# Performance work log

Measured on AMD Instinct MI355X. Metric: run time of the kernel, lower is better.

The kernel has to match this reference:

```python
import jax, jax.numpy as jnp
import numpy as np

N_NODES = 50000
N_EDGES = 1600000
D_IN = 128
D_HID = 256   # 2 * input_dims
FC1 = 256
FC2 = 256
N_ACT = 8
EPS = 1e-5


def layer_norm(x, w, b):
    mu = jnp.mean(x, axis=-1, keepdims=True)
    var = jnp.mean((x - mu) ** 2, axis=-1, keepdims=True)
    return (x - mu) * jax.lax.rsqrt(var + EPS) * w + b


def setup_inputs() -> dict:
    key = jax.random.key(0)
    ks = jax.random.split(key, 16)
    state = jax.random.normal(ks[0], (N_NODES, D_IN), dtype=jnp.float32)
    edge_index = jax.random.randint(ks[1], (2, N_EDGES), 0, N_NODES, dtype=jnp.int64)
    agent_i = 7
    # GCNConv params (glorot-ish init is fine for a numeric reference)
    conv_w = jax.random.normal(ks[2], (D_IN, D_HID), dtype=jnp.float32) / np.sqrt(D_IN)
    conv_b = jnp.zeros((D_HID,), dtype=jnp.float32)
    f1 = 1.0 / np.sqrt(D_HID)
    fc1_w = jax.random.uniform(ks[3], (D_HID, FC1), minval=-f1, maxval=f1, dtype=jnp.float32)
    fc1_b = jax.random.uniform(ks[4], (FC1,), minval=-f1, maxval=f1, dtype=jnp.float32)
    f2 = 1.0 / np.sqrt(FC1)
    fc2_w = jax.random.uniform(ks[5], (FC1, FC2), minval=-f2, maxval=f2, dtype=jnp.float32)
    fc2_b = jax.random.uniform(ks[6], (FC2,), minval=-f2, maxval=f2, dtype=jnp.float32)
    ln1_w = jnp.ones((FC1,), dtype=jnp.float32)
    ln1_b = jnp.zeros((FC1,), dtype=jnp.float32)
    ln2_w = jnp.ones((FC2,), dtype=jnp.float32)
    ln2_b = jnp.zeros((FC2,), dtype=jnp.float32)
    f3 = 0.003
    mu_w = jax.random.uniform(ks[7], (FC2, N_ACT), minval=-f3, maxval=f3, dtype=jnp.float32)
    mu_b = jax.random.uniform(ks[8], (N_ACT,), minval=-f3, maxval=f3, dtype=jnp.float32)
    return {
        "state": state, "edge_index": edge_index, "agent_i": agent_i,
        "conv_w": conv_w, "conv_b": conv_b,
        "fc1_w": fc1_w, "fc1_b": fc1_b, "ln1_w": ln1_w, "ln1_b": ln1_b,
        "fc2_w": fc2_w, "fc2_b": fc2_b, "ln2_w": ln2_w, "ln2_b": ln2_b,
        "mu_w": mu_w, "mu_b": mu_b,
    }


def gcn_conv(x, edge_index, w, b):
    N = x.shape[0]
    loops = jnp.arange(N, dtype=edge_index.dtype)
    src = jnp.concatenate([edge_index[0], loops])
    dst = jnp.concatenate([edge_index[1], loops])
    ones = jnp.ones(src.shape[0], dtype=x.dtype)
    deg = jax.ops.segment_sum(ones, dst, num_segments=N)
    dinv = jnp.where(deg > 0, jax.lax.rsqrt(deg), 0.0)
    norm = dinv[src] * dinv[dst]                        # [E+N]
    h = x @ w                                           # [N, D_HID]
    msg = h[src] * norm[:, None]                        # gather: [E+N, D_HID]
    return jax.ops.segment_sum(msg, dst, num_segments=N) + b


def reference(state, edge_index, agent_i, conv_w, conv_b,
              fc1_w, fc1_b, ln1_w, ln1_b, fc2_w, fc2_b, ln2_w, ln2_b,
              mu_w, mu_b):
    x = gcn_conv(state, edge_index, conv_w, conv_b)     # [N, D_HID]
    x = jax.nn.relu(x[agent_i])                         # [D_HID]
    x = jax.nn.relu(layer_norm(x @ fc1_w + fc1_b, ln1_w, ln1_b))
    x = jax.nn.relu(layer_norm(x @ fc2_w + fc2_b, ln2_w, ln2_b))
    return jax.nn.sigmoid(x @ mu_w + mu_b)              # [N_ACT]
```

## Files before the change

kernel.cpp:

```cpp
#include <hip/hip_runtime.h>
#include <hip/hip_bf16.h>

#define D_IN  128
#define D_HID 256
#define NB_A  256
#define NT_A  512
#define NB_B  256
#define NT_B  512
#define NT_C  512
#define MAXG  512
#define HASHN 2048
#define PBM_STRIDE 72

#define OFF_BAR  0
#define OFF_M    16
#define OFF_DEG  32
#define OFF_PBM  1024
#define OFF_CM   20480
#define OFF_MAP  21504
#define OFF_H0   24576
#define OFF_H1   25088
#define OFF_H2   25600

#define ALD(p)   __hip_atomic_load((p),      __ATOMIC_RELAXED, __HIP_MEMORY_SCOPE_AGENT)
#define AST(p,v) __hip_atomic_store((p),(v), __ATOMIC_RELAXED, __HIP_MEMORY_SCOPE_AGENT)

__device__ __forceinline__ float ldf(const void* p, long long i, bool b16) {
    if (b16) {
        unsigned short u = ((const unsigned short*)p)[i];
        return __uint_as_float(((unsigned int)u) << 16);
    }
    return ((const float*)p)[i];
}

__device__ __forceinline__ unsigned hash_n(int key) {
    return (((unsigned)key * 2654435761u) >> 21) & (HASHN - 1);
}

__device__ __forceinline__ int detect_i64(const void* edges, int tid, int* s) {
    if (tid < 64) {
        const unsigned* w = (const unsigned*)edges;
        unsigned long long b = __ballot(w[2 * tid + 1] == 0u);
        if (tid == 0) *s = (b == ~0ULL) ? 1 : 0;
    }
    __syncthreads();
    return *s;
}

__device__ __forceinline__ int detect_b16(const void* state, int tid, int* s) {
    if (tid < 64) {
        const unsigned short* p = (const unsigned short*)state;
        unsigned short v = p[tid];
        int e = (v >> 7) & 0xff;
        unsigned long long b = __ballot(v == 0 || (e >= 90 && e <= 140));
        if (tid == 0) *s = (b == ~0ULL) ? 1 : 0;
    }
    __syncthreads();
    return *s;
}

__device__ __forceinline__ void grid_bar(int* slot, int cnt, bool wait) {
    __syncthreads();
    if (threadIdx.x == 0) {
        __threadfence();
        __hip_atomic_fetch_add(slot, 1, __ATOMIC_RELEASE, __HIP_MEMORY_SCOPE_AGENT);
        if (wait) {
            while (__hip_atomic_load(slot, __ATOMIC_RELAXED, __HIP_MEMORY_SCOPE_AGENT) < cnt)
                __builtin_amdgcn_s_sleep(2);
            __threadfence();
        }
    }
    __syncthreads();
}

__global__ void __launch_bounds__(NT_A) k_A(const void* edges, const void* state,
                                            const int* agent_p,
                                            const void* w0, const void* w1,
                                            const void* w2, const void* w3,
                                            int* wsi, long long n_edges) {
    __shared__ int s_pref[NT_A];
    __shared__ int s_list[64];
    __shared__ int s_i64, s_b16;
    int tid = threadIdx.x, bid = blockIdx.x;
    int i64 = detect_i64(edges, tid, &s_i64);
    int b16 = detect_b16(state, tid, &s_b16);

    if (bid == 0) {
        if (tid < 8) AST(&wsi[OFF_BAR + tid], 0);
        for (int i = tid; i <= MAXG; i += NT_A) AST(&wsi[OFF_DEG + i], 0);
    }

    {
        int esz = b16 ? 2 : 4;
        long long gt = (long long)bid * NT_A + tid;
        const void* arr[4] = { w0, w1, w2, w3 };
        const int elems[4] = { D_IN * D_HID, D_HID * D_HID, D_HID * D_HID, D_HID * 8 };
        long long base = 0;
        #pragma unroll
        for (int a = 0; a < 4; a++) {
            long long lines = ((long long)elems[a] * esz) >> 6;
            long long idx = gt - base;
            if (idx >= 0 && idx < lines) {
                unsigned v = *(const unsigned*)((const char*)arr[a] + (idx << 6));
                asm volatile("" :: "v"(v));
            }
            base += lines;
        }
    }

    int agent = agent_p[0];
    long long base4 = ((long long)bid * NT_A + tid) * 4;
    const long long stride4 = (long long)NB_A * NT_A * 4;
    long long nv = n_edges & ~3LL;
    int c = 0;
    if (i64) {
        const long long* dst = (const long long*)edges + n_edges;
        for (long long e = base4; e < nv; e += stride4) {
            long2 a = *(const long2*)(dst + e);
            long2 b = *(const long2*)(dst + e + 2);
            c += ((int)a.x == agent) + ((int)a.y == agent)
               + ((int)b.x == agent) + ((int)b.y == agent);
        }
        if (bid == 0 && tid == 0)
            for (long long e = nv; e < n_edges; e++) c += ((int)dst[e] == agent);
    } else {
        const int* dst = (const int*)edges + n_edges;
        for (long long e = base4; e < nv; e += stride4) {
            int4 a = *(const int4*)(dst + e);
            c += (a.x == agent) + (a.y == agent) + (a.z == agent) + (a.w == agent);
        }
        if (bid == 0 && tid == 0)
            for (long long e = nv; e < n_edges; e++) c += (dst[e] == agent);
    }
    s_pref[tid] = c;
    __syncthreads();
    #pragma unroll
    for (int off = 1; off < NT_A; off <<= 1) {
        int v = (tid >= off) ? s_pref[tid - off] : 0;
        __syncthreads();
        s_pref[tid] += v;
        __syncthreads();
    }
    int excl = s_pref[tid] - c;
    int total = s_pref[NT_A - 1];
    if (c > 0 && excl < 64) {
        int k = excl;
        if (i64) {
            const long long* src = (const long long*)edges;
            const long long* dst = src + n_edges;
            for (long long e = base4; e < nv; e += stride4) {
                long2 a = *(const long2*)(dst + e);
                long2 b = *(const long2*)(dst + e + 2);
                if ((int)a.x == agent) { if (k < 64) s_list[k] = (int)src[e];     k++; }
                if ((int)a.y == agent) { if (k < 64) s_list[k] = (int)src[e + 1]; k++; }
                if ((int)b.x == agent) { if (k < 64) s_list[k] = (int)src[e + 2]; k++; }
                if ((int)b.y == agent) { if (k < 64) s_list[k] = (int)src[e + 3]; k++; }
            }
            if (bid == 0 && tid == 0)
                for (long long e = nv; e < n_edges; e++)
                    if ((int)dst[e] == agent) { if (k < 64) s_list[k] = (int)src[e]; k++; }
        } else {
            const int* src = (const int*)edges;
            const int* dst = src + n_edges;
            for (long long e = base4; e < nv; e += stride4) {
                int4 a = *(const int4*)(dst + e);
                if (a.x == agent) { if (k < 64) s_list[k] = src[e];     k++; }
                if (a.y == agent) { if (k < 64) s_list[k] = src[e + 1]; k++; }
                if (a.z == agent) { if (k < 64) s_list[k] = src[e + 2]; k++; }
                if (a.w == agent) { if (k < 64) s_list[k] = src[e + 3]; k++; }
            }
            if (bid == 0 && tid == 0)
                for (long long e = nv; e < n_edges; e++)
                    if (dst[e] == agent) { if (k < 64) s_list[k] = src[e]; k++; }
        }
    }
    __syncthreads();
    int* reg = wsi + OFF_PBM + bid * PBM_STRIDE;
    int tw = total < 64 ? total : 64;
    if (tid == 0) reg[0] = tw;
    if (tid < tw) reg[1 + tid] = s_list[tid];
}

__global__ void __launch_bounds__(NT_B) k_B(const void* edges, const int* agent_p,
                                            int* wsi, long long n_edges) {
    __shared__ int s_pref[NT_B];
    __shared__ int s_nodes[MAXG + 1];
    __shared__ int s_hkey[HASHN];
    __shared__ int s_hval[HASHN];
    __shared__ int s_cnt[MAXG + 1];
    __shared__ int s_i64, s_nu;
    int tid = threadIdx.x, bid = blockIdx.x;
    int i64 = detect_i64(edges, tid, &s_i64);

    int bc = 0;
    if (tid < NB_A) {
        bc = wsi[OFF_PBM + tid * PBM_STRIDE];
        bc = bc < 64 ? (bc < 0 ? 0 : bc) : 64;
    }
    s_pref[tid] = bc;
    __syncthreads();
    #pragma unroll
    for (int off = 1; off < NT_B; off <<= 1) {
        int v = (tid >= off) ? s_pref[tid - off] : 0;
        __syncthreads();
        s_pref[tid] += v;
        __syncthreads();
    }
    int excl = s_pref[tid] - bc;
    int mc = s_pref[NT_B - 1];
    int m = mc < MAXG ? mc : MAXG;
    if (tid < NB_A) {
        for (int i = 0; i < bc; i++) {
            int g = excl + i;
            if (g < MAXG) s_nodes[1 + g] = wsi[OFF_PBM + tid * PBM_STRIDE + 1 + i];
        }
    }
    if (tid == 0) s_nodes[0] = agent_p[0];
    for (int i = tid; i < HASHN; i += NT_B) s_hkey[i] = -1;
    for (int i = tid; i <= m; i += NT_B) s_cnt[i] = 0;
    __syncthreads();

    if (tid == 0) {
        int nu = 0;
        for (int j = 0; j <= m; j++) {
            int key = s_nodes[j];
            unsigned h = hash_n(key);
            while (true) {
                if (s_hkey[h] == -1) { s_hkey[h] = key; s_hval[h] = nu++; break; }
                if (s_hkey[h] == key) break;
                h = (h + 1) & (HASHN - 1);
            }
        }
        s_nu = nu;
    }
    __syncthreads();

    auto probe = [&](int d) {
        unsigned h = hash_n(d);
        while (true) {
            int k = s_hkey[h];
            if (k == -1) break;
            if (k == d) { atomicAdd(&s_cnt[s_hval[h]], 1); break; }
            h = (h + 1) & (HASHN - 1);
        }
    };

    long long base4 = ((long long)bid * NT_B + tid) * 4;
    const long long stride4 = (long long)NB_B * NT_B * 4;
    long long nv = n_edges & ~3LL;
    if (i64) {
        const long long* dst = (const long long*)edges + n_edges;
        for (long long e = base4; e < nv; e += stride4) {
            long2 a = *(const long2*)(dst + e);
            long2 b = *(const long2*)(dst + e + 2);
            probe((int)a.x); probe((int)a.y); probe((int)b.x); probe((int)b.y);
        }
        if (bid == 0 && tid == 0)
            for (long long e = nv; e < n_edges; e++) probe((int)dst[e]);
    } else {
        const int* dst = (const int*)edges + n_edges;
        for (long long e = base4; e < nv; e += stride4) {
            int4 a = *(const int4*)(dst + e);
            probe(a.x); probe(a.y); probe(a.z); probe(a.w);
        }
        if (bid == 0 && tid == 0)
            for (long long e = nv; e < n_edges; e++) probe(dst[e]);
    }
    __syncthreads();
    int nu = s_nu;
    for (int i = tid; i < nu; i += NT_B)
        if (s_cnt[i]) atomicAdd(&wsi[OFF_DEG + i], s_cnt[i]);
    if (bid == 0) {
        if (tid == 0) wsi[OFF_M] = m;
        for (int i = tid; i < m; i += NT_B) wsi[OFF_CM + i] = s_nodes[1 + i];
        for (int j = tid; j <= m; j += NT_B) {
            int key = s_nodes[j];
            unsigned h = hash_n(key);
            while (s_hkey[h] != key) h = (h + 1) & (HASHN - 1);
            wsi[OFF_MAP + j] = s_hval[h];
        }
    }
}

__device__ __forceinline__ float ln256(float v, const void* lnw, const void* lnb,
                                       float* s_red, int tid, bool b16) {
    if (tid < 256) {
        float x = v;
        #pragma unroll
        for (int o = 32; o > 0; o >>= 1) x += __shfl_down(x, o);
        if ((tid & 63) == 0) s_red[tid >> 6] = x;
    }
    __syncthreads();
    float mu = (s_red[0] + s_red[1] + s_red[2] + s_red[3]) * (1.0f / 256.0f);
    if (tid < 256) {
        float dd = v - mu;
        float x = dd * dd;
        #pragma unroll
        for (int o = 32; o > 0; o >>= 1) x += __shfl_down(x, o);
        if ((tid & 63) == 0) s_red[4 + (tid >> 6)] = x;
    }
    __syncthreads();
    float var = (s_red[4] + s_red[5] + s_red[6] + s_red[7]) * (1.0f / 256.0f);
    float y = 0.0f;
    if (tid < 256)
        y = fmaxf((v - mu) * rsqrtf(var + 1e-5f) * ldf(lnw, tid, b16) + ldf(lnb, tid, b16), 0.0f);
    __syncthreads();
    return y;
}

__global__ void __launch_bounds__(NT_C) k_C(
    const void* state, const int* agent_p,
    const void* conv_w, const void* conv_b,
    const void* fc1_w, const void* fc1_b, const void* ln1_w, const void* ln1_b,
    const void* fc2_w, const void* fc2_b, const void* ln2_w, const void* ln2_b,
    const void* mu_w, const void* mu_b,
    int* wsi, void* out)
{
    __shared__ float s_in[D_HID];
    __shared__ float s_part[NT_C];
    __shared__ float s_xs[D_IN];
    __shared__ float s_red[8];
    __shared__ int   s_src[MAXG];
    __shared__ float s_w[MAXG];
    __shared__ int   s_b16;

    int tid = threadIdx.x, bid = blockIdx.x;
    bool b16 = detect_b16(state, tid, &s_b16) != 0;
    float* wsf = (float*)wsi;
    int* bar = wsi + OFF_BAR;

    if (bid < 8) {
        int m = wsi[OFF_M];
        m = m < MAXG ? m : MAXG;
        int agent = agent_p[0];
        float dinv_a = rsqrtf((float)(ALD(&wsi[OFF_DEG]) + 1));
        for (int i = tid; i < m; i += NT_C) {
            s_src[i] = wsi[OFF_CM + i];
            int u = wsi[OFF_MAP + 1 + i];
            s_w[i] = dinv_a * rsqrtf((float)(ALD(&wsi[OFF_DEG + u]) + 1));
        }
        __syncthreads();
        int d = tid & 127, jg = tid >> 7;
        float acc = (jg == 0) ? dinv_a * dinv_a * ldf(state, (long long)agent * D_IN + d, b16) : 0.0f;
        for (int j = jg; j < m; j += 4)
            acc += s_w[j] * ldf(state, (long long)s_src[j] * D_IN + d, b16);
        s_part[tid] = acc;
        __syncthreads();
        if (tid < D_IN)
            s_xs[tid] = s_part[tid] + s_part[tid + 128] + s_part[tid + 256] + s_part[tid + 384];
        __syncthreads();
        int o = bid * 32 + (tid & 31), ks = tid >> 5;
        float a = 0.0f;
        #pragma unroll 8
        for (int k = ks * 8; k < ks * 8 + 8; k++)
            a += s_xs[k] * ldf(conv_w, (long long)k * D_HID + o, b16);
        s_part[tid] = a;
        __syncthreads();
        if (tid < 32) {
            int oo = bid * 32 + tid;
            float h = ldf(conv_b, oo, b16);
            #pragma unroll
            for (int s2 = 0; s2 < 16; s2++) h += s_part[s2 * 32 + tid];
            AST(&wsf[OFF_H0 + oo], fmaxf(h, 0.0f));
        }
    }
    grid_bar(&bar[0], 25, bid >= 8 && bid < 16);
    if (bid < 8) return;

    if (bid < 16) {
        if (tid < D_HID) s_in[tid] = ALD(&wsf[OFF_H0 + tid]);
        __syncthreads();
        int o = (bid - 8) * 32 + (tid & 31), ks = tid >> 5;
        float a = 0.0f;
        #pragma unroll 8
        for (int k = ks * 16; k < ks * 16 + 16; k++)
            a += s_in[k] * ldf(fc1_w, (long long)k * D_HID + o, b16);
        s_part[tid] = a;
        __syncthreads();
        if (tid < 32) {
            int oo = (bid - 8) * 32 + tid;
            float h = ldf(fc1_b, oo, b16);
            #pragma unroll
            for (int s2 = 0; s2 < 16; s2++) h += s_part[s2 * 32 + tid];
            AST(&wsf[OFF_H1 + oo], h);
        }
    }
    grid_bar(&bar[1], 17, bid >= 16 && bid < 24);
    if (bid < 16) return;

    if (bid < 24) {
        float v = (tid < D_HID) ? ALD(&wsf[OFF_H1 + tid]) : 0.0f;
        float y = ln256(v, ln1_w, ln1_b, s_red, tid, b16);
        if (tid < D_HID) s_in[tid] = y;
        __syncthreads();
        int o = (bid - 16) * 32 + (tid & 31), ks = tid >> 5;
        float a = 0.0f;
        #pragma unroll 8
        for (int k = ks * 16; k < ks * 16 + 16; k++)
            a += s_in[k] * ldf(fc2_w, (long long)k * D_HID + o, b16);
        s_part[tid] = a;
        __syncthreads();
        if (tid < 32) {
            int oo = (bid - 16) * 32 + tid;
            float h = ldf(fc2_b, oo, b16);
            #pragma unroll
            for (int s2 = 0; s2 < 16; s2++) h += s_part[s2 * 32 + tid];
            AST(&wsf[OFF_H2 + oo], h);
        }
    }
    grid_bar(&bar[2], 9, bid == 24);
    if (bid < 24) return;

    {
        float v = (tid < D_HID) ? ALD(&wsf[OFF_H2 + tid]) : 0.0f;
        float y = ln256(v, ln2_w, ln2_b, s_red, tid, b16);
        if (tid < D_HID) s_in[tid] = y;
        __syncthreads();
        int o = tid & 7, ks = tid >> 3;
        float a = 0.0f;
        #pragma unroll
        for (int k = ks * 4; k < ks * 4 + 4; k++)
            a += s_in[k] * ldf(mu_w, (long long)k * 8 + o, b16);
        s_part[tid] = a;
        __syncthreads();
        if (tid < 8) {
            float acc = ldf(mu_b, tid, b16);
            #pragma unroll
            for (int s2 = 0; s2 < 64; s2++) acc += s_part[s2 * 8 + tid];
            float r = 1.0f / (1.0f + expf(-acc));
            if (b16) ((__hip_bfloat16*)out)[tid] = __float2bfloat16(r);
            else     ((float*)out)[tid] = r;
        }
    }
}

extern "C" void kernel_launch(void* const* d_in, const int* in_sizes, int n_in,
                              void* d_out, int out_size, void* d_ws, size_t ws_size,
                              hipStream_t stream) {
    const void* state = d_in[0];
    const void* edges = d_in[1];
    const int* agent = (const int*)d_in[2];
    int* wsi = (int*)d_ws;
    long long n_edges = in_sizes[1] / 2;

    k_A<<<NB_A, NT_A, 0, stream>>>(edges, state, agent,
                                   d_in[3], d_in[5], d_in[9], d_in[13],
                                   wsi, n_edges);
    k_B<<<NB_B, NT_B, 0, stream>>>(edges, agent, wsi, n_edges);
    k_C<<<25, NT_C, 0, stream>>>(state, agent,
                                 d_in[3], d_in[4],
                                 d_in[5], d_in[6], d_in[7], d_in[8],
                                 d_in[9], d_in[10], d_in[11], d_in[12],
                                 d_in[13], d_in[14],
                                 wsi, d_out);
}
```

Measured before the change: 36.15 us.

## Fuse degree-count and MLP kernels into one launch with grid barrier

Merges the degree-counting kernel and the GCN/MLP tail kernel into a single kernel. A grid-wide barrier replaces the kernel boundary, and the first 25 blocks continue into the dense stages using the neighbour list and hash map already in shared memory. This removes one launch and the workspace round trip for the node list and map. It also prefetches the needed state rows into cache before the edge scan. The risks are a spin barrier across 256 blocks, which needs every block to be co-resident, and higher shared-memory use per block, which may lower occupancy during the edge scan.

```diff
diff --git a/kernel.cpp b/kernel.cpp
--- a/kernel.cpp
+++ b/kernel.cpp
@@ -5,19 +5,15 @@
 #define D_HID 256
 #define NB_A  256
 #define NT_A  512
-#define NB_B  256
-#define NT_B  512
-#define NT_C  512
+#define NBLK  256
+#define NTHR  512
 #define MAXG  512
 #define HASHN 2048
 #define PBM_STRIDE 72
 
 #define OFF_BAR  0
-#define OFF_M    16
 #define OFF_DEG  32
 #define OFF_PBM  1024
-#define OFF_CM   20480
-#define OFF_MAP  21504
 #define OFF_H0   24576
 #define OFF_H1   25088
 #define OFF_H2   25600
@@ -181,16 +177,58 @@
     if (tid < tw) reg[1 + tid] = s_list[tid];
 }
 
-__global__ void __launch_bounds__(NT_B) k_B(const void* edges, const int* agent_p,
-                                            int* wsi, long long n_edges) {
-    __shared__ int s_pref[NT_B];
-    __shared__ int s_nodes[MAXG + 1];
-    __shared__ int s_hkey[HASHN];
-    __shared__ int s_hval[HASHN];
-    __shared__ int s_cnt[MAXG + 1];
-    __shared__ int s_i64, s_nu;
+__device__ __forceinline__ float ln256(float v, const void* lnw, const void* lnb,
+                                       float* s_red, int tid, bool b16) {
+    if (tid < 256) {
+        float x = v;
+        #pragma unroll
+        for (int o = 32; o > 0; o >>= 1) x += __shfl_down(x, o);
+        if ((tid & 63) == 0) s_red[tid >> 6] = x;
+    }
+    __syncthreads();
+    float mu = (s_red[0] + s_red[1] + s_red[2] + s_red[3]) * (1.0f / 256.0f);
+    if (tid < 256) {
+        float dd = v - mu;
+        float x = dd * dd;
+        #pragma unroll
+        for (int o = 32; o > 0; o >>= 1) x += __shfl_down(x, o);
+        if ((tid & 63) == 0) s_red[4 + (tid >> 6)] = x;
+    }
+    __syncthreads();
+    float var = (s_red[4] + s_red[5] + s_red[6] + s_red[7]) * (1.0f / 256.0f);
+    float y = 0.0f;
+    if (tid < 256)
+        y = fmaxf((v - mu) * rsqrtf(var + 1e-5f) * ldf(lnw, tid, b16) + ldf(lnb, tid, b16), 0.0f);
+    __syncthreads();
+    return y;
+}
+
+__global__ void __launch_bounds__(NTHR) k_BC(
+    const void* state, const void* edges, const int* agent_p,
+    const void* conv_w, const void* conv_b,
+    const void* fc1_w, const void* fc1_b, const void* ln1_w, const void* ln1_b,
+    const void* fc2_w, const void* fc2_b, const void* ln2_w, const void* ln2_b,
+    const void* mu_w, const void* mu_b,
+    int* wsi, long long n_edges, void* out)
+{
+    __shared__ int   s_pref[NTHR];
+    __shared__ int   s_nodes[MAXG + 1];
+    __shared__ int   s_hkey[HASHN];
+    __shared__ int   s_hval[HASHN];
+    __shared__ int   s_cnt[MAXG + 1];
+    __shared__ float s_in[D_HID];
+    __shared__ float s_part[NTHR];
+    __shared__ float s_xs[D_IN];
+    __shared__ float s_red[8];
+    __shared__ float s_w[MAXG];
+    __shared__ int   s_i64, s_b16, s_nu;
+
     int tid = threadIdx.x, bid = blockIdx.x;
     int i64 = detect_i64(edges, tid, &s_i64);
+    bool b16 = detect_b16(state, tid, &s_b16) != 0;
+    float* wsf = (float*)wsi;
+    int* bar = wsi + OFF_BAR;
+    int agent = agent_p[0];
 
     int bc = 0;
     if (tid < NB_A) {
@@ -200,14 +238,14 @@
     s_pref[tid] = bc;
     __syncthreads();
     #pragma unroll
-    for (int off = 1; off < NT_B; off <<= 1) {
+    for (int off = 1; off < NTHR; off <<= 1) {
         int v = (tid >= off) ? s_pref[tid - off] : 0;
         __syncthreads();
         s_pref[tid] += v;
         __syncthreads();
     }
     int excl = s_pref[tid] - bc;
-    int mc = s_pref[NT_B - 1];
+    int mc = s_pref[NTHR - 1];
     int m = mc < MAXG ? mc : MAXG;
     if (tid < NB_A) {
         for (int i = 0; i < bc; i++) {
@@ -215,9 +253,9 @@
             if (g < MAXG) s_nodes[1 + g] = wsi[OFF_PBM + tid * PBM_STRIDE + 1 + i];
         }
     }
-    if (tid == 0) s_nodes[0] = agent_p[0];
-    for (int i = tid; i < HASHN; i += NT_B) s_hkey[i] = -1;
-    for (int i = tid; i <= m; i += NT_B) s_cnt[i] = 0;
+    if (tid == 0) s_nodes[0] = agent;
+    for (int i = tid; i < HASHN; i += NTHR) s_hkey[i] = -1;
+    for (int i = tid; i <= m; i += NTHR) s_cnt[i] = 0;
     __syncthreads();
 
     if (tid == 0) {
@@ -235,6 +273,17 @@
     }
     __syncthreads();
 
+    if (bid < 8) {
+        int esz = b16 ? 2 : 4;
+        int chunks = (D_IN * esz) >> 6;
+        for (int i = tid; i < (m + 1) * chunks; i += NTHR) {
+            int j = i / chunks, ch = i - j * chunks;
+            long long row = s_nodes[j];
+            unsigned v = *(const unsigned*)((const char*)state + row * D_IN * esz + ch * 64);
+            asm volatile("" :: "v"(v));
+        }
+    }
+
     auto probe = [&](int d) {
         unsigned h = hash_n(d);
         while (true) {
@@ -244,9 +293,8 @@
             h = (h + 1) & (HASHN - 1);
         }
     };
-
-    long long base4 = ((long long)bid * NT_B + tid) * 4;
-    const long long stride4 = (long long)NB_B * NT_B * 4;
+    long long base4 = ((long long)bid * NTHR + tid) * 4;
+    const long long stride4 = (long long)NBLK * NTHR * 4;
     long long nv = n_edges & ~3LL;
     if (i64) {
         const long long* dst = (const long long*)edges + n_edges;
@@ -267,83 +315,25 @@
             for (long long e = nv; e < n_edges; e++) probe(dst[e]);
     }
     __syncthreads();
-    int nu = s_nu;
-    for (int i = tid; i < nu; i += NT_B)
+    for (int i = tid; i < s_nu; i += NTHR)
         if (s_cnt[i]) atomicAdd(&wsi[OFF_DEG + i], s_cnt[i]);
-    if (bid == 0) {
-        if (tid == 0) wsi[OFF_M] = m;
-        for (int i = tid; i < m; i += NT_B) wsi[OFF_CM + i] = s_nodes[1 + i];
-        for (int j = tid; j <= m; j += NT_B) {
-            int key = s_nodes[j];
+
+    grid_bar(&bar[0], NBLK, bid < 25);
+    if (bid >= 25) return;
+
+    if (bid < 8) {
+        float dinv_a = rsqrtf((float)(ALD(&wsi[OFF_DEG]) + 1));
+        for (int i = tid; i < m; i += NTHR) {
+            int key = s_nodes[1 + i];
             unsigned h = hash_n(key);
             while (s_hkey[h] != key) h = (h + 1) & (HASHN - 1);
-            wsi[OFF_MAP + j] = s_hval[h];
-        }
-    }
-}
-
-__device__ __forceinline__ float ln256(float v, const void* lnw, const void* lnb,
-                                       float* s_red, int tid, bool b16) {
-    if (tid < 256) {
-        float x = v;
-        #pragma unroll
-        for (int o = 32; o > 0; o >>= 1) x += __shfl_down(x, o);
-        if ((tid & 63) == 0) s_red[tid >> 6] = x;
-    }
-    __syncthreads();
-    float mu = (s_red[0] + s_red[1] + s_red[2] + s_red[3]) * (1.0f / 256.0f);
-    if (tid < 256) {
-        float dd = v - mu;
-        float x = dd * dd;
-        #pragma unroll
-        for (int o = 32; o > 0; o >>= 1) x += __shfl_down(x, o);
-        if ((tid & 63) == 0) s_red[4 + (tid >> 6)] = x;
-    }
-    __syncthreads();
-    float var = (s_red[4] + s_red[5] + s_red[6] + s_red[7]) * (1.0f / 256.0f);
-    float y = 0.0f;
-    if (tid < 256)
-        y = fmaxf((v - mu) * rsqrtf(var + 1e-5f) * ldf(lnw, tid, b16) + ldf(lnb, tid, b16), 0.0f);
-    __syncthreads();
-    return y;
-}
-
-__global__ void __launch_bounds__(NT_C) k_C(
-    const void* state, const int* agent_p,
-    const void* conv_w, const void* conv_b,
-    const void* fc1_w, const void* fc1_b, const void* ln1_w, const void* ln1_b,
-    const void* fc2_w, const void* fc2_b, const void* ln2_w, const void* ln2_b,
-    const void* mu_w, const void* mu_b,
-    int* wsi, void* out)
-{
-    __shared__ float s_in[D_HID];
-    __shared__ float s_part[NT_C];
-    __shared__ float s_xs[D_IN];
-    __shared__ float s_red[8];
-    __shared__ int   s_src[MAXG];
-    __shared__ float s_w[MAXG];
-    __shared__ int   s_b16;
-
-    int tid = threadIdx.x, bid = blockIdx.x;
-    bool b16 = detect_b16(state, tid, &s_b16) != 0;
-    float* wsf = (float*)wsi;
-    int* bar = wsi + OFF_BAR;
-
-    if (bid < 8) {
-        int m = wsi[OFF_M];
-        m = m < MAXG ? m : MAXG;
-        int agent = agent_p[0];
-        float dinv_a = rsqrtf((float)(ALD(&wsi[OFF_DEG]) + 1));
-        for (int i = tid; i < m; i += NT_C) {
-            s_src[i] = wsi[OFF_CM + i];
-            int u = wsi[OFF_MAP + 1 + i];
-            s_w[i] = dinv_a * rsqrtf((float)(ALD(&wsi[OFF_DEG + u]) + 1));
+            s_w[i] = dinv_a * rsqrtf((float)(ALD(&wsi[OFF_DEG + s_hval[h]]) + 1));
         }
         __syncthreads();
         int d = tid & 127, jg = tid >> 7;
         float acc = (jg == 0) ? dinv_a * dinv_a * ldf(state, (long long)agent * D_IN + d, b16) : 0.0f;
         for (int j = jg; j < m; j += 4)
-            acc += s_w[j] * ldf(state, (long long)s_src[j] * D_IN + d, b16);
+            acc += s_w[j] * ldf(state, (long long)s_nodes[1 + j] * D_IN + d, b16);
         s_part[tid] = acc;
         __syncthreads();
         if (tid < D_IN)
@@ -364,7 +354,7 @@
             AST(&wsf[OFF_H0 + oo], fmaxf(h, 0.0f));
         }
     }
-    grid_bar(&bar[0], 25, bid >= 8 && bid < 16);
+    grid_bar(&bar[1], 25, bid >= 8 && bid < 16);
     if (bid < 8) return;
 
     if (bid < 16) {
@@ -385,7 +375,7 @@
             AST(&wsf[OFF_H1 + oo], h);
         }
     }
-    grid_bar(&bar[1], 17, bid >= 16 && bid < 24);
+    grid_bar(&bar[2], 17, bid >= 16 && bid < 24);
     if (bid < 16) return;
 
     if (bid < 24) {
@@ -408,7 +398,7 @@
             AST(&wsf[OFF_H2 + oo], h);
         }
     }
-    grid_bar(&bar[2], 9, bid == 24);
+    grid_bar(&bar[3], 9, bid == 24);
     if (bid < 24) return;
 
     {
@@ -446,11 +436,10 @@
     k_A<<<NB_A, NT_A, 0, stream>>>(edges, state, agent,
                                    d_in[3], d_in[5], d_in[9], d_in[13],
                                    wsi, n_edges);
-    k_B<<<NB_B, NT_B, 0, stream>>>(edges, agent, wsi, n_edges);
-    k_C<<<25, NT_C, 0, stream>>>(state, agent,
-                                 d_in[3], d_in[4],
-                                 d_in[5], d_in[6], d_in[7], d_in[8],
-                                 d_in[9], d_in[10], d_in[11], d_in[12],
-                                 d_in[13], d_in[14],
-                                 wsi, d_out);
-}
+    k_BC<<<NBLK, NTHR, 0, stream>>>(state, edges, agent,
+                                    d_in[3], d_in[4],
+                                    d_in[5], d_in[6], d_in[7], d_in[8],
+                                    d_in[9], d_in[10], d_in[11], d_in[12],
+                                    d_in[13], d_in[14],
+                                    wsi, n_edges, d_out);
+}
```

New measurement: 40.24 us. 1.11x slower.

## Prefetch per-stage weights into LDS and split grid barrier into arrive/wait

Applied to the files above, without the earlier changes.

In the tail kernel, each block now loads its slice of conv/fc1/fc2/mu weights into shared memory before waiting on the previous stage, so weight fetches overlap the upstream chain. The grid barrier is split into arrive and wait so each stage waits only on the 8 producer blocks of the previous stage, not on all blocks. The edge-scan loops in the first two kernels now process 8 edges per thread per iteration instead of 4, to raise memory-level parallelism. This adds 32KB of LDS per block and extra scalar loads in the collection pass.

```diff
diff --git a/kernel.cpp b/kernel.cpp
--- a/kernel.cpp
+++ b/kernel.cpp
@@ -59,16 +59,19 @@
     return *s;
 }
 
-__device__ __forceinline__ void grid_bar(int* slot, int cnt, bool wait) {
+__device__ __forceinline__ void bar_arrive(int* slot) {
     __syncthreads();
     if (threadIdx.x == 0) {
         __threadfence();
         __hip_atomic_fetch_add(slot, 1, __ATOMIC_RELEASE, __HIP_MEMORY_SCOPE_AGENT);
-        if (wait) {
-            while (__hip_atomic_load(slot, __ATOMIC_RELAXED, __HIP_MEMORY_SCOPE_AGENT) < cnt)
-                __builtin_amdgcn_s_sleep(2);
-            __threadfence();
-        }
+    }
+}
+
+__device__ __forceinline__ void bar_wait(int* slot, int cnt) {
+    if (threadIdx.x == 0) {
+        while (__hip_atomic_load(slot, __ATOMIC_RELAXED, __HIP_MEMORY_SCOPE_AGENT) < cnt)
+            __builtin_amdgcn_s_sleep(2);
+        __threadfence();
     }
     __syncthreads();
 }
@@ -109,25 +112,31 @@
     }
 
     int agent = agent_p[0];
-    long long base4 = ((long long)bid * NT_A + tid) * 4;
-    const long long stride4 = (long long)NB_A * NT_A * 4;
-    long long nv = n_edges & ~3LL;
+    long long base8 = ((long long)bid * NT_A + tid) * 8;
+    const long long stride8 = (long long)NB_A * NT_A * 8;
+    long long nv = n_edges & ~7LL;
     int c = 0;
     if (i64) {
         const long long* dst = (const long long*)edges + n_edges;
-        for (long long e = base4; e < nv; e += stride4) {
-            long2 a = *(const long2*)(dst + e);
-            long2 b = *(const long2*)(dst + e + 2);
-            c += ((int)a.x == agent) + ((int)a.y == agent)
-               + ((int)b.x == agent) + ((int)b.y == agent);
+        for (long long e = base8; e < nv; e += stride8) {
+            long2 a0 = *(const long2*)(dst + e);
+            long2 a1 = *(const long2*)(dst + e + 2);
+            long2 a2 = *(const long2*)(dst + e + 4);
+            long2 a3 = *(const long2*)(dst + e + 6);
+            c += ((int)a0.x == agent) + ((int)a0.y == agent)
+               + ((int)a1.x == agent) + ((int)a1.y == agent)
+               + ((int)a2.x == agent) + ((int)a2.y == agent)
+               + ((int)a3.x == agent) + ((int)a3.y == agent);
         }
         if (bid == 0 && tid == 0)
             for (long long e = nv; e < n_edges; e++) c += ((int)dst[e] == agent);
     } else {
         const int* dst = (const int*)edges + n_edges;
-        for (long long e = base4; e < nv; e += stride4) {
+        for (long long e = base8; e < nv; e += stride8) {
             int4 a = *(const int4*)(dst + e);
-            c += (a.x == agent) + (a.y == agent) + (a.z == agent) + (a.w == agent);
+            int4 b = *(const int4*)(dst + e + 4);
+            c += (a.x == agent) + (a.y == agent) + (a.z == agent) + (a.w == agent)
+               + (b.x == agent) + (b.y == agent) + (b.z == agent) + (b.w == agent);
         }
         if (bid == 0 && tid == 0)
             for (long long e = nv; e < n_edges; e++) c += (dst[e] == agent);
@@ -148,13 +157,11 @@
         if (i64) {
             const long long* src = (const long long*)edges;
             const long long* dst = src + n_edges;
-            for (long long e = base4; e < nv; e += stride4) {
-                long2 a = *(const long2*)(dst + e);
-                long2 b = *(const long2*)(dst + e + 2);
-                if ((int)a.x == agent) { if (k < 64) s_list[k] = (int)src[e];     k++; }
-                if ((int)a.y == agent) { if (k < 64) s_list[k] = (int)src[e + 1]; k++; }
-                if ((int)b.x == agent) { if (k < 64) s_list[k] = (int)src[e + 2]; k++; }
-                if ((int)b.y == agent) { if (k < 64) s_list[k] = (int)src[e + 3]; k++; }
+            for (long long e = base8; e < nv; e += stride8) {
+                #pragma unroll
+                for (int q = 0; q < 8; q++) {
+                    if ((int)dst[e + q] == agent) { if (k < 64) s_list[k] = (int)src[e + q]; k++; }
+                }
             }
             if (bid == 0 && tid == 0)
                 for (long long e = nv; e < n_edges; e++)
@@ -162,12 +169,11 @@
         } else {
             const int* src = (const int*)edges;
             const int* dst = src + n_edges;
-            for (long long e = base4; e < nv; e += stride4) {
-                int4 a = *(const int4*)(dst + e);
-                if (a.x == agent) { if (k < 64) s_list[k] = src[e];     k++; }
-                if (a.y == agent) { if (k < 64) s_list[k] = src[e + 1]; k++; }
-                if (a.z == agent) { if (k < 64) s_list[k] = src[e + 2]; k++; }
-                if (a.w == agent) { if (k < 64) s_list[k] = src[e + 3]; k++; }
+            for (long long e = base8; e < nv; e += stride8) {
+                #pragma unroll
+                for (int q = 0; q < 8; q++) {
+                    if (dst[e + q] == agent) { if (k < 64) s_list[k] = src[e + q]; k++; }
+                }
             }
             if (bid == 0 && tid == 0)
                 for (long long e = nv; e < n_edges; e++)
@@ -245,23 +251,28 @@
         }
     };
 
-    long long base4 = ((long long)bid * NT_B + tid) * 4;
-    const long long stride4 = (long long)NB_B * NT_B * 4;
-    long long nv = n_edges & ~3LL;
+    long long base8 = ((long long)bid * NT_B + tid) * 8;
+    const long long stride8 = (long long)NB_B * NT_B * 8;
+    long long nv = n_edges & ~7LL;
     if (i64) {
         const long long* dst = (const long long*)edges + n_edges;
-        for (long long e = base4; e < nv; e += stride4) {
-            long2 a = *(const long2*)(dst + e);
-            long2 b = *(const long2*)(dst + e + 2);
-            probe((int)a.x); probe((int)a.y); probe((int)b.x); probe((int)b.y);
+        for (long long e = base8; e < nv; e += stride8) {
+            long2 a0 = *(const long2*)(dst + e);
+            long2 a1 = *(const long2*)(dst + e + 2);
+            long2 a2 = *(const long2*)(dst + e + 4);
+            long2 a3 = *(const long2*)(dst + e + 6);
+            probe((int)a0.x); probe((int)a0.y); probe((int)a1.x); probe((int)a1.y);
+            probe((int)a2.x); probe((int)a2.y); probe((int)a3.x); probe((int)a3.y);
         }
         if (bid == 0 && tid == 0)
             for (long long e = nv; e < n_edges; e++) probe((int)dst[e]);
     } else {
         const int* dst = (const int*)edges + n_edges;
-        for (long long e = base4; e < nv; e += stride4) {
+        for (long long e = base8; e < nv; e += stride8) {
             int4 a = *(const int4*)(dst + e);
+            int4 b = *(const int4*)(dst + e + 4);
             probe(a.x); probe(a.y); probe(a.z); probe(a.w);
+            probe(b.x); probe(b.y); probe(b.z); probe(b.w);
         }
         if (bid == 0 && tid == 0)
             for (long long e = nv; e < n_edges; e++) probe(dst[e]);
@@ -316,6 +327,7 @@
     const void* mu_w, const void* mu_b,
     int* wsi, void* out)
 {
+    __shared__ float s_wl[8192];
     __shared__ float s_in[D_HID];
     __shared__ float s_part[NT_C];
     __shared__ float s_xs[D_IN];
@@ -328,6 +340,23 @@
     bool b16 = detect_b16(state, tid, &s_b16) != 0;
     float* wsf = (float*)wsi;
     int* bar = wsi + OFF_BAR;
+
+    if (bid < 8) {
+        int o0 = bid * 32;
+        for (int i = tid; i < D_IN * 32; i += NT_C)
+            s_wl[i] = ldf(conv_w, (long long)(i >> 5) * D_HID + o0 + (i & 31), b16);
+    } else if (bid < 16) {
+        int o0 = (bid - 8) * 32;
+        for (int i = tid; i < D_HID * 32; i += NT_C)
+            s_wl[i] = ldf(fc1_w, (long long)(i >> 5) * D_HID + o0 + (i & 31), b16);
+    } else if (bid < 24) {
+        int o0 = (bid - 16) * 32;
+        for (int i = tid; i < D_HID * 32; i += NT_C)
+            s_wl[i] = ldf(fc2_w, (long long)(i >> 5) * D_HID + o0 + (i & 31), b16);
+    } else {
+        for (int i = tid; i < D_HID * 8; i += NT_C)
+            s_wl[i] = ldf(mu_w, i, b16);
+    }
 
     if (bid < 8) {
         int m = wsi[OFF_M];
@@ -349,11 +378,11 @@
         if (tid < D_IN)
             s_xs[tid] = s_part[tid] + s_part[tid + 128] + s_part[tid + 256] + s_part[tid + 384];
         __syncthreads();
-        int o = bid * 32 + (tid & 31), ks = tid >> 5;
+        int c = tid & 31, ks = tid >> 5;
         float a = 0.0f;
         #pragma unroll 8
         for (int k = ks * 8; k < ks * 8 + 8; k++)
-            a += s_xs[k] * ldf(conv_w, (long long)k * D_HID + o, b16);
+            a += s_xs[k] * s_wl[k * 32 + c];
         s_part[tid] = a;
         __syncthreads();
         if (tid < 32) {
@@ -363,18 +392,19 @@
             for (int s2 = 0; s2 < 16; s2++) h += s_part[s2 * 32 + tid];
             AST(&wsf[OFF_H0 + oo], fmaxf(h, 0.0f));
         }
-    }
-    grid_bar(&bar[0], 25, bid >= 8 && bid < 16);
-    if (bid < 8) return;
+        bar_arrive(&bar[0]);
+        return;
+    }
 
     if (bid < 16) {
+        bar_wait(&bar[0], 8);
         if (tid < D_HID) s_in[tid] = ALD(&wsf[OFF_H0 + tid]);
         __syncthreads();
-        int o = (bid - 8) * 32 + (tid & 31), ks = tid >> 5;
+        int c = tid & 31, ks = tid >> 5;
         float a = 0.0f;
         #pragma unroll 8
         for (int k = ks * 16; k < ks * 16 + 16; k++)
-            a += s_in[k] * ldf(fc1_w, (long long)k * D_HID + o, b16);
+            a += s_in[k] * s_wl[k * 32 + c];
         s_part[tid] = a;
         __syncthreads();
         if (tid < 32) {
@@ -384,20 +414,21 @@
             for (int s2 = 0; s2 < 16; s2++) h += s_part[s2 * 32 + tid];
             AST(&wsf[OFF_H1 + oo], h);
         }
-    }
-    grid_bar(&bar[1], 17, bid >= 16 && bid < 24);
-    if (bid < 16) return;
+        bar_arrive(&bar[1]);
+        return;
+    }
 
     if (bid < 24) {
+        bar_wait(&bar[1], 8);
         float v = (tid < D_HID) ? ALD(&wsf[OFF_H1 + tid]) : 0.0f;
         float y = ln256(v, ln1_w, ln1_b, s_red, tid, b16);
         if (tid < D_HID) s_in[tid] = y;
         __syncthreads();
-        int o = (bid - 16) * 32 + (tid & 31), ks = tid >> 5;
+        int c = tid & 31, ks = tid >> 5;
         float a = 0.0f;
         #pragma unroll 8
         for (int k = ks * 16; k < ks * 16 + 16; k++)
-            a += s_in[k] * ldf(fc2_w, (long long)k * D_HID + o, b16);
+            a += s_in[k] * s_wl[k * 32 + c];
         s_part[tid] = a;
         __syncthreads();
         if (tid < 32) {
@@ -407,11 +438,12 @@
             for (int s2 = 0; s2 < 16; s2++) h += s_part[s2 * 32 + tid];
             AST(&wsf[OFF_H2 + oo], h);
         }
-    }
-    grid_bar(&bar[2], 9, bid == 24);
-    if (bid < 24) return;
+        bar_arrive(&bar[2]);
+        return;
+    }
 
     {
+        bar_wait(&bar[2], 8);
         float v = (tid < D_HID) ? ALD(&wsf[OFF_H2 + tid]) : 0.0f;
         float y = ln256(v, ln2_w, ln2_b, s_red, tid, b16);
         if (tid < D_HID) s_in[tid] = y;
@@ -420,7 +452,7 @@
         float a = 0.0f;
         #pragma unroll
         for (int k = ks * 4; k < ks * 4 + 4; k++)
-            a += s_in[k] * ldf(mu_w, (long long)k * 8 + o, b16);
+            a += s_in[k] * s_wl[k * 8 + o];
         s_part[tid] = a;
         __syncthreads();
         if (tid < 8) {
```

Measured after the change: 35.96 us. No clear change (-0.5%).
